# Optimization experiments

Hardware: AMD Instinct MI355X
Metric: run time of the kernel (lower is better)

The kernel has to match this reference:

```python
import jax, jax.numpy as jnp
import numpy as np

B, C, LF = 64, 256, 32
H = W = LF  # required: H = W = att_dilation*(LF-1)+1 with att_dilation=1
C1 = 256    # conv1_outchannel


def setup_inputs() -> dict:
    key = jax.random.key(0)
    k0, k1, k2 = jax.random.split(key, 3)
    x = jax.random.normal(k0, (B, C, H, W), jnp.float32)
    conv1_w = jax.random.normal(k1, (C1, C, 7, 7), jnp.float32) * 0.02
    conv1_b = jnp.zeros((C1,), jnp.float32)
    bn1_g = jnp.ones((C1,), jnp.float32)
    bn1_b = jnp.zeros((C1,), jnp.float32)
    conv2_w = jax.random.normal(k2, (LF * LF, C1, 1, 1), jnp.float32) * 0.02
    conv2_b = jnp.zeros((LF * LF,), jnp.float32)
    bn2_g = jnp.ones((LF * LF,), jnp.float32)
    bn2_b = jnp.zeros((LF * LF,), jnp.float32)
    return {"x": x, "conv1_w": conv1_w, "conv1_b": conv1_b, "bn1_g": bn1_g,
            "bn1_b": bn1_b, "conv2_w": conv2_w, "conv2_b": conv2_b,
            "bn2_g": bn2_g, "bn2_b": bn2_b}


def _bn(h, g, b, eps=1e-5):
    # training-mode BatchNorm2d: biased batch stats over (N,H,W)
    m = h.mean(axis=(0, 2, 3), keepdims=True)
    v = jnp.var(h, axis=(0, 2, 3), keepdims=True)
    return g[None, :, None, None] * (h - m) * jax.lax.rsqrt(v + eps) + b[None, :, None, None]


def reference(x, conv1_w, conv1_b, bn1_g, bn1_b, conv2_w, conv2_b, bn2_g, bn2_b):
    dn = ('NCHW', 'OIHW', 'NCHW')
    # conv1: 7x7, dilation 2, 'same' padding (=6)
    h = jax.lax.conv_general_dilated(x, conv1_w, (1, 1), ((6, 6), (6, 6)),
                                     rhs_dilation=(2, 2), dimension_numbers=dn)
    h = _bn(h + conv1_b[None, :, None, None], bn1_g, bn1_b)
    # conv_last: 1x1 -> LF^2 channels
    k = jax.lax.conv_general_dilated(h, conv2_w, (1, 1), ((0, 0), (0, 0)),
                                     dimension_numbers=dn)
    k = _bn(k + conv2_b[None, :, None, None], bn2_g, bn2_b)
    k = jax.nn.softmax(k, axis=1)                 # [B, LF*LF, H, W]
    kmap = k.reshape(B, LF, LF, H, W)             # per-pixel LFxLF window weights
    # conv3d-with-groups=B hack == per-pixel weighted sum over the whole LFxLF map:
    # y[b,i,j,c] = sum_{u,v} kmap[b,u,v,i,j] * x[b,c,u,v]
    y = jnp.einsum('buvij,bcuv->bijc', kmap, x)   # [B, H, W, C]
    # torch.reshape of [1, B*H*W, C, 1, 1] to (B, C, H, W): raw row-major reinterpret
    return y.reshape(B, C, H, W)
```

## Files before the change

kernel.cpp:

```cpp
#include <hip/hip_runtime.h>

typedef unsigned short u16;
typedef unsigned int u32;
typedef short bf16x8 __attribute__((ext_vector_type(8)));
typedef float f32x4 __attribute__((ext_vector_type(4)));

#define NB   64
#define NC   256
#define NO   256
#define NM   1024
#define PW   44
#define PPIX 1936

__device__ __forceinline__ u16 f2bf(float f) {
    u32 u = __builtin_bit_cast(u32, f);
    u32 r = (u + 0x7FFFu + ((u >> 16) & 1u)) >> 16;
    return (u16)r;
}
__device__ __forceinline__ void ld16(const void* g, void* l) {
    __builtin_amdgcn_global_load_lds((const __attribute__((address_space(1))) u32*)g,
                                     (__attribute__((address_space(3))) u32*)l, 16, 0, 0);
}

#define VMCNT(n) { asm volatile("s_waitcnt vmcnt(" #n ")" ::: "memory"); __builtin_amdgcn_sched_barrier(0); }
#define LGKM(n)  { asm volatile("s_waitcnt lgkmcnt(" #n ")" ::: "memory"); __builtin_amdgcn_sched_barrier(0); }

__global__ __launch_bounds__(256) void k_transpose_pad(const float* __restrict__ x, u16* __restrict__ xp) {
    __shared__ u16 tile[64 * 65];
    const int b = blockIdx.z, ij0 = blockIdx.x * 64, c0 = blockIdx.y * 64;
    const int tid = threadIdx.x;
#pragma unroll
    for (int it = 0; it < 16; ++it) {
        int idx = it * 256 + tid;
        int cr = idx >> 6, ijr = idx & 63;
        tile[ijr * 65 + cr] = f2bf(x[((size_t)(b * NC + c0 + cr) << 10) + ij0 + ijr]);
    }
    __syncthreads();
#pragma unroll
    for (int it = 0; it < 16; ++it) {
        int idx = it * 256 + tid;
        int ijr = idx >> 6, cr = idx & 63;
        int pix = ij0 + ijr;
        int i = pix >> 5, j = pix & 31;
        int prow = (i + 6) * PW + (j + 6);
        xp[((size_t)(b * PPIX + prow) << 8) + c0 + cr] = tile[ijr * 65 + cr];
    }
}

__global__ __launch_bounds__(256) void k_w1prep(const float* __restrict__ w1, u16* __restrict__ w1t) {
    const int o = blockIdx.x, c = threadIdx.x;
    const float* src = w1 + ((size_t)(o * NC + c)) * 49;
#pragma unroll
    for (int t = 0; t < 49; ++t)
        w1t[((size_t)(t * NO + o) << 8) + c] = f2bf(src[t]);
}

__global__ __launch_bounds__(512, 1) void k_conv1(const u16* __restrict__ xp, const u16* __restrict__ w1t,
                                                  u16* __restrict__ h, float* __restrict__ s1, float* __restrict__ q1) {
    __shared__ u16 lsA[4 * 256 * 32];
    __shared__ u16 lsB[4 * 256 * 32];
    const int tid = threadIdx.x, wv = tid >> 6, lane = tid & 63;
    const int wm = wv & 1, wn = wv >> 1;
    const int bb = blockIdx.z, ij0 = blockIdx.x * 256;

    f32x4 acc[8][4] = {};
    bf16x8 aX[8], bX[4], aY[8], bY[4];

    const int lc8 = (((tid & 3) ^ ((tid >> 3) & 3)) << 3);
    int aRow[2], bRow[2], dstO[2];
#pragma unroll
    for (int c = 0; c < 2; ++c) {
        int r = (c << 7) + (tid >> 2);
        int pix = ij0 + r, i = pix >> 5, j = pix & 31;
        aRow[c] = ((bb * PPIX + i * PW + j) << 8) + lc8;
        bRow[c] = (r << 8) + lc8;
        dstO[c] = ((c << 7) + (wv << 4)) << 5;
    }
    const int chsw = (((lane >> 4) ^ (((lane & 15) >> 1) & 3)) << 3);
    const u16* pA0 = lsA + (((wm << 7) + (lane & 15)) << 5) + chsw;
    const u16* pB0 = lsB + (((wn << 6) + (lane & 15)) << 5) + chsw;

    int sp = 0, sq = 0, stap = 0, sci = 0, skh = 0, sreg = 0;
    auto STAGE = [&]() {
        const int toff = (((sp << 1) * PW + (sq << 1)) << 8) + (sci << 6) + (skh << 5);
        const int woff = (stap << 16) + (sci << 6) + (skh << 5);
        u16* dA = (u16*)lsA + (sreg << 13);
        u16* dB = (u16*)lsB + (sreg << 13);
#pragma unroll
        for (int c = 0; c < 2; ++c) ld16(xp + aRow[c] + toff, dA + dstO[c]);
#pragma unroll
        for (int c = 0; c < 2; ++c) ld16(w1t + bRow[c] + woff, dB + dstO[c]);
        sreg = (sreg + 1) & 3;
        skh ^= 1;
        if (!skh) {
            ++stap; ++sq;
            if (sq == 7) { sq = 0; ++sp; }
            if (stap == 49) { stap = 0; sp = 0; sq = 0; ++sci; }
        }
    };
    auto RD = [&](int v, bf16x8 (&a)[8], bf16x8 (&b)[4]) {
        const int rb = (v & 3) << 13;
        const u16* pA = pA0 + rb;
        const u16* pB = pB0 + rb;
#pragma unroll
        for (int fi = 0; fi < 8; ++fi) a[fi] = *(const bf16x8*)(pA + (fi << 9));
#pragma unroll
        for (int fj = 0; fj < 4; ++fj) b[fj] = *(const bf16x8*)(pB + (fj << 9));
    };
    auto MM = [&](bf16x8 (&a)[8], bf16x8 (&b)[4]) {
        __builtin_amdgcn_s_setprio(1);
#pragma unroll
        for (int fi = 0; fi < 8; ++fi)
#pragma unroll
            for (int fj = 0; fj < 4; ++fj)
                acc[fi][fj] = __builtin_amdgcn_mfma_f32_16x16x32_bf16(a[fi], b[fj], acc[fi][fj], 0, 0, 0);
        __builtin_amdgcn_s_setprio(0);
    };

    STAGE(); STAGE(); STAGE();
    VMCNT(8);
    __builtin_amdgcn_s_barrier();
    RD(0, aX, bX);

#pragma unroll 1
    for (int u = 0; u < 388; u += 2) {
        VMCNT(4);
        __builtin_amdgcn_s_barrier();
        RD(u + 1, aY, bY);
        STAGE();
        LGKM(12);
        MM(aX, bX);

        VMCNT(4);
        __builtin_amdgcn_s_barrier();
        RD(u + 2, aX, bX);
        STAGE();
        LGKM(12);
        MM(aY, bY);
    }
    VMCNT(4);
    __builtin_amdgcn_s_barrier();
    RD(389, aY, bY);
    STAGE();
    LGKM(12);
    MM(aX, bX);

    VMCNT(4);
    __builtin_amdgcn_s_barrier();
    RD(390, aX, bX);
    LGKM(12);
    MM(aY, bY);

    VMCNT(0);
    __builtin_amdgcn_s_barrier();
    RD(391, aY, bY);
    LGKM(12);
    MM(aX, bX);

    LGKM(0);
    MM(aY, bY);

    const int colb = (wn << 6) + (lane & 15);
    const int rowb = ij0 + (wm << 7) + ((lane >> 4) << 2);
#pragma unroll
    for (int fj = 0; fj < 4; ++fj) {
        const int col = colb + (fj << 4);
        float s = 0.f, qq = 0.f;
#pragma unroll
        for (int fi = 0; fi < 8; ++fi) {
            const int row = rowb + (fi << 4);
#pragma unroll
            for (int v = 0; v < 4; ++v) {
                float val = acc[fi][fj][v];
                h[((size_t)((bb << 10) + row + v) << 8) + col] = f2bf(val);
                s += val; qq += val * val;
            }
        }
        s += __shfl_xor(s, 16);  s += __shfl_xor(s, 32);
        qq += __shfl_xor(qq, 16); qq += __shfl_xor(qq, 32);
        if (lane < 16) { atomicAdd(&s1[col], s); atomicAdd(&q1[col], qq); }
    }
}

__global__ void k_bn1fin(const float* __restrict__ s1, const float* __restrict__ q1,
                         const float* __restrict__ g1, float* __restrict__ a1) {
    const int o = threadIdx.x;
    float mean = s1[o] * (1.f / 65536.f);
    float var  = fmaxf(q1[o] * (1.f / 65536.f) - mean * mean, 0.f);
    a1[o] = g1[o] * rsqrtf(var + 1e-5f);
}

__global__ __launch_bounds__(256) void k_fold2(const float* __restrict__ w2, const float* __restrict__ a1,
                                               u16* __restrict__ w2s) {
    const int m = blockIdx.x, c = threadIdx.x;
    size_t idx = ((size_t)m << 8) + c;
    w2s[idx] = f2bf(w2[idx] * a1[c]);
}

__global__ __launch_bounds__(256) void k_conv2(const u16* __restrict__ h, const u16* __restrict__ w2s,
                                               u16* __restrict__ kb, float* __restrict__ s2, float* __restrict__ q2) {
    __shared__ u16 lsA[128 * 32];
    __shared__ u16 lsB[128 * 32];
    const int tid = threadIdx.x, wv = tid >> 6, lane = tid & 63;
    const int wm = wv & 1, wn = wv >> 1;
    const int bb = blockIdx.z, ij0 = blockIdx.x * 128, m0 = blockIdx.y * 128;

    f32x4 acc[4][4] = {};
    const int lr = lane >> 2, lc8 = (lane & 3) << 3;
    int arow[2], brw[2];
    u16 *dA[2], *dB[2];
#pragma unroll
    for (int u = 0; u < 2; ++u) {
        int r = (wv << 5) + (u << 4) + lr;
        arow[u] = (((bb << 10) + ij0 + r) << 8) + lc8;
        brw[u]  = ((m0 + r) << 8) + lc8;
        dA[u] = lsA + (((wv << 5) + (u << 4)) << 5);
        dB[u] = lsB + (((wv << 5) + (u << 4)) << 5);
    }
    const u16* pA0 = lsA + (((wm << 6) + (lane & 15)) << 5) + ((lane >> 4) << 3);
    const u16* pB0 = lsB + (((wn << 6) + (lane & 15)) << 5) + ((lane >> 4) << 3);

    for (int s = 0; s < 8; ++s) {
        const int cc = s << 5;
#pragma unroll
        for (int u = 0; u < 2; ++u) {
            ld16(h + arow[u] + cc, dA[u]);
            ld16(w2s + brw[u] + cc, dB[u]);
        }
        __syncthreads();
        bf16x8 af[4], bv[4];
#pragma unroll
        for (int f = 0; f < 4; ++f) af[f] = *(const bf16x8*)(pA0 + (f << 9));
#pragma unroll
        for (int f = 0; f < 4; ++f) bv[f] = *(const bf16x8*)(pB0 + (f << 9));
#pragma unroll
        for (int fi = 0; fi < 4; ++fi)
#pragma unroll
            for (int fj = 0; fj < 4; ++fj)
                acc[fi][fj] = __builtin_amdgcn_mfma_f32_16x16x32_bf16(af[fi], bv[fj], acc[fi][fj], 0, 0, 0);
        __syncthreads();
    }
    const int colb = m0 + (wn << 6) + (lane & 15);
    const int rowb = ij0 + (wm << 6) + ((lane >> 4) << 2);
#pragma unroll
    for (int fj = 0; fj < 4; ++fj) {
        const int col = colb + (fj << 4);
        float s = 0.f, qq = 0.f;
#pragma unroll
        for (int fi = 0; fi < 4; ++fi) {
            const int row = rowb + (fi << 4);
#pragma unroll
            for (int v = 0; v < 4; ++v) {
                float val = acc[fi][fj][v];
                kb[((size_t)((bb << 10) + row + v) << 10) + col] = f2bf(val);
                s += val; qq += val * val;
            }
        }
        s += __shfl_xor(s, 16);  s += __shfl_xor(s, 32);
        qq += __shfl_xor(qq, 16); qq += __shfl_xor(qq, 32);
        if (lane < 16) { atomicAdd(&s2[col], s); atomicAdd(&q2[col], qq); }
    }
}

__global__ void k_bn2fin(const float* __restrict__ s2, const float* __restrict__ q2,
                         const float* __restrict__ g2, const float* __restrict__ b2,
                         float* __restrict__ a2, float* __restrict__ b2f) {
    const int m = blockIdx.x * 256 + threadIdx.x;
    float mean = s2[m] * (1.f / 65536.f);
    float var  = fmaxf(q2[m] * (1.f / 65536.f) - mean * mean, 0.f);
    float a = g2[m] * rsqrtf(var + 1e-5f);
    a2[m] = a;
    b2f[m] = b2[m] - mean * a;
}

__global__ __launch_bounds__(256) void k_softmax(u16* __restrict__ kb,
                                                 const float* __restrict__ a2, const float* __restrict__ b2f) {
    __shared__ float redm[4], reds[4];
    const int row = (blockIdx.y << 10) + blockIdx.x;
    u16* base = kb + ((size_t)row << 10);
    const int tid = threadIdx.x, lane = tid & 63, wv = tid >> 6;
    const int m0 = tid << 2;
    uint2 rw = *(const uint2*)(base + m0);
    float u[4];
    u[0] = __builtin_bit_cast(float, (rw.x & 0xFFFFu) << 16);
    u[1] = __builtin_bit_cast(float, rw.x & 0xFFFF0000u);
    u[2] = __builtin_bit_cast(float, (rw.y & 0xFFFFu) << 16);
    u[3] = __builtin_bit_cast(float, rw.y & 0xFFFF0000u);
#pragma unroll
    for (int i = 0; i < 4; ++i) u[i] = a2[m0 + i] * u[i] + b2f[m0 + i];
    float mx = fmaxf(fmaxf(u[0], u[1]), fmaxf(u[2], u[3]));
#pragma unroll
    for (int off = 32; off; off >>= 1) mx = fmaxf(mx, __shfl_xor(mx, off));
    if (lane == 0) redm[wv] = mx;
    __syncthreads();
    mx = fmaxf(fmaxf(redm[0], redm[1]), fmaxf(redm[2], redm[3]));
    float e[4], s = 0.f;
#pragma unroll
    for (int i = 0; i < 4; ++i) { e[i] = __expf(u[i] - mx); s += e[i]; }
#pragma unroll
    for (int off = 32; off; off >>= 1) s += __shfl_xor(s, off);
    if (lane == 0) reds[wv] = s;
    __syncthreads();
    float inv = 1.f / (reds[0] + reds[1] + reds[2] + reds[3]);
    u32 o0 = (u32)f2bf(e[0] * inv) | ((u32)f2bf(e[1] * inv) << 16);
    u32 o1 = (u32)f2bf(e[2] * inv) | ((u32)f2bf(e[3] * inv) << 16);
    *(uint2*)(base + m0) = make_uint2(o0, o1);
}

__global__ __launch_bounds__(256) void k_final(const u16* __restrict__ ksm, const float* __restrict__ x,
                                               float* __restrict__ out) {
    __shared__ u16 lsA[128 * 32];
    __shared__ u16 lsB[128 * 32];
    const int tid = threadIdx.x, wv = tid >> 6, lane = tid & 63;
    const int wm = wv & 1, wn = wv >> 1;
    const int bb = blockIdx.z, ij0 = blockIdx.x * 128, c0 = blockIdx.y * 128;

    f32x4 acc[4][4] = {};
    const int lr = lane >> 2, lc8 = (lane & 3) << 3;
    int arow[2], brw[2];
    u16 *dA[2], *sB[2];
#pragma unroll
    for (int u = 0; u < 2; ++u) {
        int r = (wv << 5) + (u << 4) + lr;
        arow[u] = (((bb << 10) + ij0 + r) << 10) + lc8;
        brw[u]  = (((bb << 8) + c0 + r) << 10) + lc8;
        dA[u] = lsA + (((wv << 5) + (u << 4)) << 5);
        sB[u] = lsB + (((wv << 5) + (u << 4) + lr) << 5) + lc8;
    }
    const u16* pA0 = lsA + (((wm << 6) + (lane & 15)) << 5) + ((lane >> 4) << 3);
    const u16* pB0 = lsB + (((wn << 6) + (lane & 15)) << 5) + ((lane >> 4) << 3);

    for (int s = 0; s < 32; ++s) {
        const int cc = s << 5;
#pragma unroll
        for (int u = 0; u < 2; ++u) ld16(ksm + arow[u] + cc, dA[u]);
        float4 f00 = *(const float4*)(x + brw[0] + cc);
        float4 f01 = *(const float4*)(x + brw[0] + cc + 4);
        float4 f10 = *(const float4*)(x + brw[1] + cc);
        float4 f11 = *(const float4*)(x + brw[1] + cc + 4);
        uint4 vb0, vb1;
        vb0.x = (u32)f2bf(f00.x) | ((u32)f2bf(f00.y) << 16);
        vb0.y = (u32)f2bf(f00.z) | ((u32)f2bf(f00.w) << 16);
        vb0.z = (u32)f2bf(f01.x) | ((u32)f2bf(f01.y) << 16);
        vb0.w = (u32)f2bf(f01.z) | ((u32)f2bf(f01.w) << 16);
        vb1.x = (u32)f2bf(f10.x) | ((u32)f2bf(f10.y) << 16);
        vb1.y = (u32)f2bf(f10.z) | ((u32)f2bf(f10.w) << 16);
        vb1.z = (u32)f2bf(f11.x) | ((u32)f2bf(f11.y) << 16);
        vb1.w = (u32)f2bf(f11.z) | ((u32)f2bf(f11.w) << 16);
        *(uint4*)sB[0] = vb0;
        *(uint4*)sB[1] = vb1;
        __syncthreads();
        bf16x8 af[4], bv[4];
#pragma unroll
        for (int f = 0; f < 4; ++f) af[f] = *(const bf16x8*)(pA0 + (f << 9));
#pragma unroll
        for (int f = 0; f < 4; ++f) bv[f] = *(const bf16x8*)(pB0 + (f << 9));
#pragma unroll
        for (int fi = 0; fi < 4; ++fi)
#pragma unroll
            for (int fj = 0; fj < 4; ++fj)
                acc[fi][fj] = __builtin_amdgcn_mfma_f32_16x16x32_bf16(af[fi], bv[fj], acc[fi][fj], 0, 0, 0);
        __syncthreads();
    }
    const int colb = c0 + (wn << 6) + (lane & 15);
    const int rowb = ij0 + (wm << 6) + ((lane >> 4) << 2);
#pragma unroll
    for (int fi = 0; fi < 4; ++fi) {
        const int row = rowb + (fi << 4);
#pragma unroll
        for (int fj = 0; fj < 4; ++fj) {
            const int col = colb + (fj << 4);
#pragma unroll
            for (int v = 0; v < 4; ++v)
                out[((size_t)((bb << 10) + row + v) << 8) + col] = acc[fi][fj][v];
        }
    }
}

extern "C" void kernel_launch(void* const* d_in, const int* in_sizes, int n_in,
                              void* d_out, int out_size, void* d_ws, size_t ws_size,
                              hipStream_t stream) {
    const float* x  = (const float*)d_in[0];
    const float* w1 = (const float*)d_in[1];
    const float* g1 = (const float*)d_in[3];
    const float* w2 = (const float*)d_in[5];
    const float* g2 = (const float*)d_in[7];
    const float* b2 = (const float*)d_in[8];
    float* out = (float*)d_out;
    char* ws = (char*)d_ws;

    u16* xp  = (u16*)ws;
    u16* kb  = (u16*)ws;
    u16* h   = (u16*)(ws + 134217728);
    u16* w1t = (u16*)(ws + 134217728 + 33554432);
    u16* w2s = w1t;
    char* sm = ws + 134217728 + 33554432 + 6422528;
    float* s1  = (float*)(sm);
    float* q1  = (float*)(sm + 1024);
    float* s2  = (float*)(sm + 2048);
    float* q2  = (float*)(sm + 6144);
    float* a1  = (float*)(sm + 10240);
    float* a2  = (float*)(sm + 14336);
    float* b2f = (float*)(sm + 18432);

    hipMemsetAsync(sm, 0, 10240, stream);
    hipMemsetAsync(xp, 0, (size_t)NB * PPIX * 256 * 2, stream);
    k_transpose_pad<<<dim3(16, 4, NB), 256, 0, stream>>>(x, xp);
    k_w1prep<<<dim3(256), 256, 0, stream>>>(w1, w1t);
    k_conv1<<<dim3(4, 1, NB), 512, 0, stream>>>(xp, w1t, h, s1, q1);
    k_bn1fin<<<dim3(1), 256, 0, stream>>>(s1, q1, g1, a1);
    k_fold2<<<dim3(1024), 256, 0, stream>>>(w2, a1, w2s);
    k_conv2<<<dim3(8, 8, NB), 256, 0, stream>>>(h, w2s, kb, s2, q2);
    k_bn2fin<<<dim3(4), 256, 0, stream>>>(s2, q2, g2, b2, a2, b2f);
    k_softmax<<<dim3(1024, NB), 256, 0, stream>>>(kb, a2, b2f);
    k_final<<<dim3(8, 2, NB), 256, 0, stream>>>(kb, x, out);
}
```

Baseline: 715.3 us.

## Pipeline conv2 with 4-stage LDS ring and fuse softmax apply into final GEMM

conv2 becomes a 256x256-tile, 512-thread kernel with a 4-deep asynchronous LDS ring, swizzled LDS reads, double-buffered register fragments and MFMA priority hints. The softmax pass no longer rewrites kb; it only stores each row's max and inverse sum. k_final then recomputes exp(a2*k+b2f-max)*inv on the fly while loading its A tile, and covers all 256 channels per block with swizzled LDS. This removes one full read-modify-write pass over the large kb buffer and speeds up the conv2 GEMM, at the cost of recomputing the exp inside the final GEMM and putting the row statistics in the workspace region that h occupied.

Result: faster. 673.7 us (-5.8%).

```diff
diff --git a/kernel.cpp b/kernel.cpp
--- a/kernel.cpp
+++ b/kernel.cpp
@@ -16,6 +16,9 @@
     u32 u = __builtin_bit_cast(u32, f);
     u32 r = (u + 0x7FFFu + ((u >> 16) & 1u)) >> 16;
     return (u16)r;
+}
+__device__ __forceinline__ float bf2f(u32 lo16) {
+    return __builtin_bit_cast(float, lo16 << 16);
 }
 __device__ __forceinline__ void ld16(const void* g, void* l) {
     __builtin_amdgcn_global_load_lds((const __attribute__((address_space(1))) u32*)g,
@@ -197,57 +200,114 @@
     w2s[idx] = f2bf(w2[idx] * a1[c]);
 }
 
-__global__ __launch_bounds__(256) void k_conv2(const u16* __restrict__ h, const u16* __restrict__ w2s,
-                                               u16* __restrict__ kb, float* __restrict__ s2, float* __restrict__ q2) {
-    __shared__ u16 lsA[128 * 32];
-    __shared__ u16 lsB[128 * 32];
+__global__ __launch_bounds__(512, 1) void k_conv2(const u16* __restrict__ h, const u16* __restrict__ w2s,
+                                                  u16* __restrict__ kb, float* __restrict__ s2, float* __restrict__ q2) {
+    __shared__ u16 lsA[4 * 256 * 32];
+    __shared__ u16 lsB[4 * 256 * 32];
     const int tid = threadIdx.x, wv = tid >> 6, lane = tid & 63;
     const int wm = wv & 1, wn = wv >> 1;
-    const int bb = blockIdx.z, ij0 = blockIdx.x * 128, m0 = blockIdx.y * 128;
-
-    f32x4 acc[4][4] = {};
-    const int lr = lane >> 2, lc8 = (lane & 3) << 3;
-    int arow[2], brw[2];
-    u16 *dA[2], *dB[2];
-#pragma unroll
-    for (int u = 0; u < 2; ++u) {
-        int r = (wv << 5) + (u << 4) + lr;
-        arow[u] = (((bb << 10) + ij0 + r) << 8) + lc8;
-        brw[u]  = ((m0 + r) << 8) + lc8;
-        dA[u] = lsA + (((wv << 5) + (u << 4)) << 5);
-        dB[u] = lsB + (((wv << 5) + (u << 4)) << 5);
-    }
-    const u16* pA0 = lsA + (((wm << 6) + (lane & 15)) << 5) + ((lane >> 4) << 3);
-    const u16* pB0 = lsB + (((wn << 6) + (lane & 15)) << 5) + ((lane >> 4) << 3);
-
-    for (int s = 0; s < 8; ++s) {
-        const int cc = s << 5;
-#pragma unroll
-        for (int u = 0; u < 2; ++u) {
-            ld16(h + arow[u] + cc, dA[u]);
-            ld16(w2s + brw[u] + cc, dB[u]);
-        }
-        __syncthreads();
-        bf16x8 af[4], bv[4];
-#pragma unroll
-        for (int f = 0; f < 4; ++f) af[f] = *(const bf16x8*)(pA0 + (f << 9));
-#pragma unroll
-        for (int f = 0; f < 4; ++f) bv[f] = *(const bf16x8*)(pB0 + (f << 9));
-#pragma unroll
-        for (int fi = 0; fi < 4; ++fi)
+    const int bid = blockIdx.x;
+    const int bb = bid & 63, r2 = bid >> 6;
+    const int ij0 = (r2 >> 2) << 8, m0 = (r2 & 3) << 8;
+
+    f32x4 acc[8][4] = {};
+    bf16x8 aX[8], bX[4], aY[8], bY[4];
+
+    const int lc8 = (((tid & 3) ^ ((tid >> 3) & 3)) << 3);
+    int aRow[2], bRow[2], dstO[2];
+#pragma unroll
+    for (int c = 0; c < 2; ++c) {
+        int rr = (c << 7) + (tid >> 2);
+        aRow[c] = (((bb << 10) + ij0 + rr) << 8) + lc8;
+        bRow[c] = ((m0 + rr) << 8) + lc8;
+        dstO[c] = ((c << 7) + (wv << 4)) << 5;
+    }
+    const int chsw = (((lane >> 4) ^ (((lane & 15) >> 1) & 3)) << 3);
+    const u16* pA0 = lsA + (((wm << 7) + (lane & 15)) << 5) + chsw;
+    const u16* pB0 = lsB + (((wn << 6) + (lane & 15)) << 5) + chsw;
+
+    int sk = 0, sreg = 0;
+    auto STAGE = [&]() {
+        const int off = sk << 5;
+        u16* dA = (u16*)lsA + (sreg << 13);
+        u16* dB = (u16*)lsB + (sreg << 13);
+#pragma unroll
+        for (int c = 0; c < 2; ++c) ld16(h + aRow[c] + off, dA + dstO[c]);
+#pragma unroll
+        for (int c = 0; c < 2; ++c) ld16(w2s + bRow[c] + off, dB + dstO[c]);
+        sreg = (sreg + 1) & 3;
+        ++sk;
+    };
+    auto RD = [&](int v, bf16x8 (&a)[8], bf16x8 (&b)[4]) {
+        const int rb = (v & 3) << 13;
+        const u16* pA = pA0 + rb;
+        const u16* pB = pB0 + rb;
+#pragma unroll
+        for (int fi = 0; fi < 8; ++fi) a[fi] = *(const bf16x8*)(pA + (fi << 9));
+#pragma unroll
+        for (int fj = 0; fj < 4; ++fj) b[fj] = *(const bf16x8*)(pB + (fj << 9));
+    };
+    auto MM = [&](bf16x8 (&a)[8], bf16x8 (&b)[4]) {
+        __builtin_amdgcn_s_setprio(1);
+#pragma unroll
+        for (int fi = 0; fi < 8; ++fi)
 #pragma unroll
             for (int fj = 0; fj < 4; ++fj)
-                acc[fi][fj] = __builtin_amdgcn_mfma_f32_16x16x32_bf16(af[fi], bv[fj], acc[fi][fj], 0, 0, 0);
-        __syncthreads();
-    }
+                acc[fi][fj] = __builtin_amdgcn_mfma_f32_16x16x32_bf16(a[fi], b[fj], acc[fi][fj], 0, 0, 0);
+        __builtin_amdgcn_s_setprio(0);
+    };
+
+    STAGE(); STAGE(); STAGE();
+    VMCNT(8);
+    __builtin_amdgcn_s_barrier();
+    RD(0, aX, bX);
+
+#pragma unroll 1
+    for (int u = 0; u < 4; u += 2) {
+        VMCNT(4);
+        __builtin_amdgcn_s_barrier();
+        RD(u + 1, aY, bY);
+        STAGE();
+        LGKM(12);
+        MM(aX, bX);
+
+        VMCNT(4);
+        __builtin_amdgcn_s_barrier();
+        RD(u + 2, aX, bX);
+        STAGE();
+        LGKM(12);
+        MM(aY, bY);
+    }
+    VMCNT(4);
+    __builtin_amdgcn_s_barrier();
+    RD(5, aY, bY);
+    STAGE();
+    LGKM(12);
+    MM(aX, bX);
+
+    VMCNT(4);
+    __builtin_amdgcn_s_barrier();
+    RD(6, aX, bX);
+    LGKM(12);
+    MM(aY, bY);
+
+    VMCNT(0);
+    __builtin_amdgcn_s_barrier();
+    RD(7, aY, bY);
+    LGKM(12);
+    MM(aX, bX);
+
+    LGKM(0);
+    MM(aY, bY);
+
     const int colb = m0 + (wn << 6) + (lane & 15);
-    const int rowb = ij0 + (wm << 6) + ((lane >> 4) << 2);
+    const int rowb = ij0 + (wm << 7) + ((lane >> 4) << 2);
 #pragma unroll
     for (int fj = 0; fj < 4; ++fj) {
         const int col = colb + (fj << 4);
         float s = 0.f, qq = 0.f;
 #pragma unroll
-        for (int fi = 0; fi < 4; ++fi) {
+        for (int fi = 0; fi < 8; ++fi) {
             const int row = rowb + (fi << 4);
 #pragma unroll
             for (int v = 0; v < 4; ++v) {
@@ -273,18 +333,19 @@
     b2f[m] = b2[m] - mean * a;
 }
 
-__global__ __launch_bounds__(256) void k_softmax(u16* __restrict__ kb,
-                                                 const float* __restrict__ a2, const float* __restrict__ b2f) {
+__global__ __launch_bounds__(256) void k_rowstat(const u16* __restrict__ kb,
+                                                 const float* __restrict__ a2, const float* __restrict__ b2f,
+                                                 float* __restrict__ rowmx, float* __restrict__ rowinv) {
     __shared__ float redm[4], reds[4];
     const int row = (blockIdx.y << 10) + blockIdx.x;
-    u16* base = kb + ((size_t)row << 10);
+    const u16* base = kb + ((size_t)row << 10);
     const int tid = threadIdx.x, lane = tid & 63, wv = tid >> 6;
     const int m0 = tid << 2;
     uint2 rw = *(const uint2*)(base + m0);
     float u[4];
-    u[0] = __builtin_bit_cast(float, (rw.x & 0xFFFFu) << 16);
+    u[0] = bf2f(rw.x & 0xFFFFu);
     u[1] = __builtin_bit_cast(float, rw.x & 0xFFFF0000u);
-    u[2] = __builtin_bit_cast(float, (rw.y & 0xFFFFu) << 16);
+    u[2] = bf2f(rw.y & 0xFFFFu);
     u[3] = __builtin_bit_cast(float, rw.y & 0xFFFF0000u);
 #pragma unroll
     for (int i = 0; i < 4; ++i) u[i] = a2[m0 + i] * u[i] + b2f[m0 + i];
@@ -294,61 +355,90 @@
     if (lane == 0) redm[wv] = mx;
     __syncthreads();
     mx = fmaxf(fmaxf(redm[0], redm[1]), fmaxf(redm[2], redm[3]));
-    float e[4], s = 0.f;
-#pragma unroll
-    for (int i = 0; i < 4; ++i) { e[i] = __expf(u[i] - mx); s += e[i]; }
+    float s = 0.f;
+#pragma unroll
+    for (int i = 0; i < 4; ++i) s += __expf(u[i] - mx);
 #pragma unroll
     for (int off = 32; off; off >>= 1) s += __shfl_xor(s, off);
     if (lane == 0) reds[wv] = s;
     __syncthreads();
-    float inv = 1.f / (reds[0] + reds[1] + reds[2] + reds[3]);
-    u32 o0 = (u32)f2bf(e[0] * inv) | ((u32)f2bf(e[1] * inv) << 16);
-    u32 o1 = (u32)f2bf(e[2] * inv) | ((u32)f2bf(e[3] * inv) << 16);
-    *(uint2*)(base + m0) = make_uint2(o0, o1);
-}
-
-__global__ __launch_bounds__(256) void k_final(const u16* __restrict__ ksm, const float* __restrict__ x,
-                                               float* __restrict__ out) {
+    if (tid == 0) {
+        rowmx[row] = mx;
+        rowinv[row] = 1.f / (reds[0] + reds[1] + reds[2] + reds[3]);
+    }
+}
+
+__global__ __launch_bounds__(512, 2) void k_final(const u16* __restrict__ kb, const float* __restrict__ x,
+                                                  const float* __restrict__ a2, const float* __restrict__ b2f,
+                                                  const float* __restrict__ rowmx, const float* __restrict__ rowinv,
+                                                  float* __restrict__ out) {
     __shared__ u16 lsA[128 * 32];
-    __shared__ u16 lsB[128 * 32];
+    __shared__ u16 lsB[256 * 32];
     const int tid = threadIdx.x, wv = tid >> 6, lane = tid & 63;
-    const int wm = wv & 1, wn = wv >> 1;
-    const int bb = blockIdx.z, ij0 = blockIdx.x * 128, c0 = blockIdx.y * 128;
+    const int wm = wv >> 2, wn = wv & 3;
+    const int bid = blockIdx.x;
+    const int bb = bid & 63, ij0 = (bid >> 6) << 7;
 
     f32x4 acc[4][4] = {};
-    const int lr = lane >> 2, lc8 = (lane & 3) << 3;
-    int arow[2], brw[2];
-    u16 *dA[2], *sB[2];
-#pragma unroll
-    for (int u = 0; u < 2; ++u) {
-        int r = (wv << 5) + (u << 4) + lr;
-        arow[u] = (((bb << 10) + ij0 + r) << 10) + lc8;
-        brw[u]  = (((bb << 8) + c0 + r) << 10) + lc8;
-        dA[u] = lsA + (((wv << 5) + (u << 4)) << 5);
-        sB[u] = lsB + (((wv << 5) + (u << 4) + lr) << 5) + lc8;
-    }
-    const u16* pA0 = lsA + (((wm << 6) + (lane & 15)) << 5) + ((lane >> 4) << 3);
-    const u16* pB0 = lsB + (((wn << 6) + (lane & 15)) << 5) + ((lane >> 4) << 3);
-
+
+    const int ar = tid >> 2, am8 = (tid & 3) << 3;
+    const size_t aGlb = (((size_t)((bb << 10) + ij0 + ar)) << 10) + am8;
+    u16* aLds = (u16*)lsA + (ar << 5) + (((tid & 3) ^ ((ar >> 1) & 3)) << 3);
+    const float mxr = rowmx[(bb << 10) + ij0 + ar];
+    const float invr = rowinv[(bb << 10) + ij0 + ar];
+    const int br = tid >> 1, bm16 = (tid & 1) << 4;
+    const size_t bGlb = (((size_t)((bb << 8) + br)) << 10) + bm16;
+    const int bswz = (br >> 1) & 3;
+    u16* bLds0 = (u16*)lsB + (br << 5) + (((((tid & 1) << 1) | 0) ^ bswz) << 3);
+    u16* bLds1 = (u16*)lsB + (br << 5) + (((((tid & 1) << 1) | 1) ^ bswz) << 3);
+    const int chsw = (((lane >> 4) ^ (((lane & 15) >> 1) & 3)) << 3);
+    const u16* pA0 = lsA + (((wm << 6) + (lane & 15)) << 5) + chsw;
+    const u16* pB0 = lsB + (((wn << 6) + (lane & 15)) << 5) + chsw;
+
+#pragma unroll 1
     for (int s = 0; s < 32; ++s) {
         const int cc = s << 5;
-#pragma unroll
-        for (int u = 0; u < 2; ++u) ld16(ksm + arow[u] + cc, dA[u]);
-        float4 f00 = *(const float4*)(x + brw[0] + cc);
-        float4 f01 = *(const float4*)(x + brw[0] + cc + 4);
-        float4 f10 = *(const float4*)(x + brw[1] + cc);
-        float4 f11 = *(const float4*)(x + brw[1] + cc + 4);
-        uint4 vb0, vb1;
-        vb0.x = (u32)f2bf(f00.x) | ((u32)f2bf(f00.y) << 16);
-        vb0.y = (u32)f2bf(f00.z) | ((u32)f2bf(f00.w) << 16);
-        vb0.z = (u32)f2bf(f01.x) | ((u32)f2bf(f01.y) << 16);
-        vb0.w = (u32)f2bf(f01.z) | ((u32)f2bf(f01.w) << 16);
-        vb1.x = (u32)f2bf(f10.x) | ((u32)f2bf(f10.y) << 16);
-        vb1.y = (u32)f2bf(f10.z) | ((u32)f2bf(f10.w) << 16);
-        vb1.z = (u32)f2bf(f11.x) | ((u32)f2bf(f11.y) << 16);
-        vb1.w = (u32)f2bf(f11.z) | ((u32)f2bf(f11.w) << 16);
-        *(uint4*)sB[0] = vb0;
-        *(uint4*)sB[1] = vb1;
+        uint4 av = *(const uint4*)(kb + aGlb + cc);
+        float4 xb0 = *(const float4*)(x + bGlb + cc);
+        float4 xb1 = *(const float4*)(x + bGlb + cc + 4);
+        float4 xb2 = *(const float4*)(x + bGlb + cc + 8);
+        float4 xb3 = *(const float4*)(x + bGlb + cc + 12);
+        float4 a2lo = *(const float4*)(a2 + cc + am8);
+        float4 a2hi = *(const float4*)(a2 + cc + am8 + 4);
+        float4 bflo = *(const float4*)(b2f + cc + am8);
+        float4 bfhi = *(const float4*)(b2f + cc + am8 + 4);
+        float va[8];
+        va[0] = bf2f(av.x & 0xFFFFu); va[1] = __builtin_bit_cast(float, av.x & 0xFFFF0000u);
+        va[2] = bf2f(av.y & 0xFFFFu); va[3] = __builtin_bit_cast(float, av.y & 0xFFFF0000u);
+        va[4] = bf2f(av.z & 0xFFFFu); va[5] = __builtin_bit_cast(float, av.z & 0xFFFF0000u);
+        va[6] = bf2f(av.w & 0xFFFFu); va[7] = __builtin_bit_cast(float, av.w & 0xFFFF0000u);
+        float p[8];
+        p[0] = __expf(a2lo.x * va[0] + bflo.x - mxr) * invr;
+        p[1] = __expf(a2lo.y * va[1] + bflo.y - mxr) * invr;
+        p[2] = __expf(a2lo.z * va[2] + bflo.z - mxr) * invr;
+        p[3] = __expf(a2lo.w * va[3] + bflo.w - mxr) * invr;
+        p[4] = __expf(a2hi.x * va[4] + bfhi.x - mxr) * invr;
+        p[5] = __expf(a2hi.y * va[5] + bfhi.y - mxr) * invr;
+        p[6] = __expf(a2hi.z * va[6] + bfhi.z - mxr) * invr;
+        p[7] = __expf(a2hi.w * va[7] + bfhi.w - mxr) * invr;
+        uint4 pa;
+        pa.x = (u32)f2bf(p[0]) | ((u32)f2bf(p[1]) << 16);
+        pa.y = (u32)f2bf(p[2]) | ((u32)f2bf(p[3]) << 16);
+        pa.z = (u32)f2bf(p[4]) | ((u32)f2bf(p[5]) << 16);
+        pa.w = (u32)f2bf(p[6]) | ((u32)f2bf(p[7]) << 16);
+        uint4 pb0, pb1;
+        pb0.x = (u32)f2bf(xb0.x) | ((u32)f2bf(xb0.y) << 16);
+        pb0.y = (u32)f2bf(xb0.z) | ((u32)f2bf(xb0.w) << 16);
+        pb0.z = (u32)f2bf(xb1.x) | ((u32)f2bf(xb1.y) << 16);
+        pb0.w = (u32)f2bf(xb1.z) | ((u32)f2bf(xb1.w) << 16);
+        pb1.x = (u32)f2bf(xb2.x) | ((u32)f2bf(xb2.y) << 16);
+        pb1.y = (u32)f2bf(xb2.z) | ((u32)f2bf(xb2.w) << 16);
+        pb1.z = (u32)f2bf(xb3.x) | ((u32)f2bf(xb3.y) << 16);
+        pb1.w = (u32)f2bf(xb3.z) | ((u32)f2bf(xb3.w) << 16);
+        __syncthreads();
+        *(uint4*)aLds = pa;
+        *(uint4*)bLds0 = pb0;
+        *(uint4*)bLds1 = pb1;
         __syncthreads();
         bf16x8 af[4], bv[4];
 #pragma unroll
@@ -360,9 +450,8 @@
 #pragma unroll
             for (int fj = 0; fj < 4; ++fj)
                 acc[fi][fj] = __builtin_amdgcn_mfma_f32_16x16x32_bf16(af[fi], bv[fj], acc[fi][fj], 0, 0, 0);
-        __syncthreads();
-    }
-    const int colb = c0 + (wn << 6) + (lane & 15);
+    }
+    const int colb = (wn << 6) + (lane & 15);
     const int rowb = ij0 + (wm << 6) + ((lane >> 4) << 2);
 #pragma unroll
     for (int fi = 0; fi < 4; ++fi) {
@@ -392,6 +481,8 @@
     u16* xp  = (u16*)ws;
     u16* kb  = (u16*)ws;
     u16* h   = (u16*)(ws + 134217728);
+    float* rowmx  = (float*)(ws + 134217728);
+    float* rowinv = rowmx + 65536;
     u16* w1t = (u16*)(ws + 134217728 + 33554432);
     u16* w2s = w1t;
     char* sm = ws + 134217728 + 33554432 + 6422528;
@@ -410,8 +501,8 @@
     k_conv1<<<dim3(4, 1, NB), 512, 0, stream>>>(xp, w1t, h, s1, q1);
     k_bn1fin<<<dim3(1), 256, 0, stream>>>(s1, q1, g1, a1);
     k_fold2<<<dim3(1024), 256, 0, stream>>>(w2, a1, w2s);
-    k_conv2<<<dim3(8, 8, NB), 256, 0, stream>>>(h, w2s, kb, s2, q2);
+    k_conv2<<<dim3(1024), 512, 0, stream>>>(h, w2s, kb, s2, q2);
     k_bn2fin<<<dim3(4), 256, 0, stream>>>(s2, q2, g2, b2, a2, b2f);
-    k_softmax<<<dim3(1024, NB), 256, 0, stream>>>(kb, a2, b2f);
-    k_final<<<dim3(8, 2, NB), 256, 0, stream>>>(kb, x, out);
-}
+    k_rowstat<<<dim3(1024, NB), 256, 0, stream>>>(kb, a2, b2f, rowmx, rowinv);
+    k_final<<<dim3(512), 512, 0, stream>>>(kb, x, a2, b2f, rowmx, rowinv, out);
+}
```
